# Optimization experiments

Measured on AMD Instinct MI355X. Metric: run time of the kernel, lower is better.

## Reference

```python
import jax, jax.numpy as jnp
import numpy as np
import math

B, N, E, D = 4, 8192, 1024, 64

def setup_inputs() -> dict:
    key = jax.random.key(0)
    kx, kq, kk, kv, ko = jax.random.split(key, 5)
    x = jax.random.normal(kx, (B, N, E), dtype=jnp.float32)
    # ImplicitLinear weights: hash-generated Rademacher-like values scaled by 1/sqrt(in_features).
    # We stand in with sign(normal) * scale, matching the statistics of v_mask_generative * scale.
    wq = jnp.sign(jax.random.normal(kq, (D, E), dtype=jnp.float32)) / math.sqrt(E)
    wk = jnp.sign(jax.random.normal(kk, (D, E), dtype=jnp.float32)) / math.sqrt(E)
    wv = jnp.sign(jax.random.normal(kv, (D, E), dtype=jnp.float32)) / math.sqrt(E)
    wo = jnp.sign(jax.random.normal(ko, (E, D), dtype=jnp.float32)) / math.sqrt(D)
    return {"x": x, "wq": wq, "wk": wk, "wv": wv, "wo": wo}

def reference(x, wq, wk, wv, wo):
    # Projections: ImplicitLinear computes x @ W.T with W shaped [out, in]
    Q = jnp.einsum('bne,de->bnd', x, wq)   # [B,N,D]
    K = jnp.einsum('bne,de->bnd', x, wk)   # [B,N,D]
    V = jnp.einsum('bne,de->bnd', x, wv)   # [B,N,D]
    # ground mode: linear attention, energy = K^T @ V  -> [B,D,D]
    energy = jnp.einsum('bnd,bne->bde', K, V)
    context = jnp.einsum('bnd,bde->bne', Q, energy)  # [B,N,D]
    context = context * jnp.asarray(math.sqrt(3.0 / D), dtype=context.dtype)
    out = jnp.einsum('bnd,ed->bne', context, wo)  # [B,N,E]
    return out
```

## Files before the change

kernel.cpp:

```cpp
#include <hip/hip_runtime.h>
#include <hip/hip_bf16.h>
#include <stdint.h>


typedef __bf16 bf16x8 __attribute__((ext_vector_type(8)));
typedef float  f32x4  __attribute__((ext_vector_type(4)));

#define MFMA_BF16(A, Bb, C) __builtin_amdgcn_mfma_f32_16x16x32_bf16(A, Bb, C, 0, 0, 0)

__device__ __forceinline__ int swz8(int row, int slot) { return (slot ^ (row & 7)) << 3; }

__device__ __forceinline__ void lds_barrier() {
    asm volatile("s_waitcnt lgkmcnt(0)" ::: "memory");
    __builtin_amdgcn_s_barrier();
}

__global__ __launch_bounds__(128) void prep_kernel(
    const float* __restrict__ wq, const float* __restrict__ wk,
    const float* __restrict__ wv, const float* __restrict__ wo,
    __bf16* __restrict__ Wb)
{
    const int gid = blockIdx.x * 128 + threadIdx.x;
    const int e0  = gid * 8;
    const float* src = (e0 < 65536)  ? wq + e0
                     : (e0 < 131072) ? wk + (e0 - 65536)
                     : (e0 < 196608) ? wv + (e0 - 131072)
                                     : wo + (e0 - 196608);
    float w[8];
    *(float4*)&w[0] = *(const float4*)(src);
    *(float4*)&w[4] = *(const float4*)(src + 4);
    bf16x8 wb;
#pragma unroll
    for (int j = 0; j < 8; ++j) wb[j] = (__bf16)w[j];
    *(bf16x8*)&Wb[e0] = wb;
}

__global__ __launch_bounds__(256) void qkv_kernel(
    const float* __restrict__ x, const __bf16* __restrict__ Wb,
    float* __restrict__ Qf, float* __restrict__ Kf, float* __restrict__ Vf)
{
    __shared__ __bf16 xh[2][32 * 64];
    __shared__ __bf16 xl[2][32 * 64];

    const int tid  = threadIdx.x;
    const int lane = tid & 63;
    const int wid  = tid >> 6;
    const int lr   = lane & 15;
    const int kg   = lane >> 4;
    const int row0 = blockIdx.x * 32;
    const int sr   = tid >> 3;
    const int f8   = tid & 7;

    f32x4 acc[2][3];
#pragma unroll
    for (int i = 0; i < 2; ++i)
#pragma unroll
        for (int j = 0; j < 3; ++j) acc[i][j] = (f32x4){0.f, 0.f, 0.f, 0.f};

    const float* xbase = &x[(size_t)(row0 + sr) * 1024 + f8 * 8];
    float xv[8], xn[8], xm[8];
#pragma unroll
    for (int j = 0; j < 8; ++j) xm[j] = 0.f;

#define LOAD_X(dst, stp)                                                       \
    {                                                                          \
        *(float4*)&dst[0] = *(const float4*)(xbase + (stp) * 64);              \
        *(float4*)&dst[4] = *(const float4*)(xbase + (stp) * 64 + 4);          \
    }

    LOAD_X(xv, 0);
    LOAD_X(xn, 1);

    for (int step = 0; step < 16; ++step) {
        const int cur = step & 1;
        {
            bf16x8 h, l;
#pragma unroll
            for (int j = 0; j < 8; ++j) {
                const float v = xv[j];
                const unsigned int bb = __float_as_uint(v);
                h[j] = __builtin_bit_cast(__bf16, (unsigned short)(bb >> 16));
                l[j] = (__bf16)(v - __uint_as_float(bb & 0xffff0000u));
            }
            const int off = sr * 64 + swz8(sr, f8);
            *(bf16x8*)&xh[cur][off] = h;
            *(bf16x8*)&xl[cur][off] = l;
        }
        lds_barrier();
        if (step < 14) LOAD_X(xm, step + 2);

#pragma unroll
        for (int ks = 0; ks < 2; ++ks) {
            const int slot = ks * 4 + kg;
            bf16x8 Ah[2], Al[2], Bw[3];
#pragma unroll
            for (int bn = 0; bn < 3; ++bn) {
                const int col = wid * 48 + bn * 16 + lr;
                Bw[bn] = *(const bf16x8*)&Wb[(size_t)col * 1024 + step * 64 + slot * 8];
            }
#pragma unroll
            for (int am = 0; am < 2; ++am) {
                const int row = am * 16 + lr;
                Ah[am] = *(const bf16x8*)&xh[cur][row * 64 + swz8(row, slot)];
                Al[am] = *(const bf16x8*)&xl[cur][row * 64 + swz8(row, slot)];
            }
#pragma unroll
            for (int am = 0; am < 2; ++am)
#pragma unroll
                for (int bn = 0; bn < 3; ++bn) {
                    acc[am][bn] = MFMA_BF16(Ah[am], Bw[bn], acc[am][bn]);
                    acc[am][bn] = MFMA_BF16(Al[am], Bw[bn], acc[am][bn]);
                }
        }
#pragma unroll
        for (int j = 0; j < 8; ++j) { xv[j] = xn[j]; xn[j] = xm[j]; }
    }
#undef LOAD_X

#pragma unroll
    for (int am = 0; am < 2; ++am)
#pragma unroll
        for (int bn = 0; bn < 3; ++bn) {
            const int col  = wid * 48 + bn * 16 + lr;
            const int rowb = row0 + am * 16 + kg * 4;
            float* dst = (col < 64) ? Qf : (col < 128) ? Kf : Vf;
            const int cc = col & 63;
#pragma unroll
            for (int r = 0; r < 4; ++r)
                dst[(size_t)(rowb + r) * 64 + cc] = acc[am][bn][r];
        }
}

__global__ __launch_bounds__(256) void energy_partial_kernel(
    const float* __restrict__ Kf, const float* __restrict__ Vf,
    float* __restrict__ part)
{
    __shared__ float lK[64 * 64];
    __shared__ float lV[64 * 64];
    const int tid  = threadIdx.x;
    const int row0 = blockIdx.x * 64;

#pragma unroll
    for (int i = 0; i < 4; ++i) {
        const int idx = tid + i * 256;
        const int r   = idx >> 4;
        const int c4  = (idx & 15) << 2;
        *(float4*)&lK[r * 64 + c4] = *(const float4*)&Kf[(size_t)(row0 + r) * 64 + c4];
        *(float4*)&lV[r * 64 + c4] = *(const float4*)&Vf[(size_t)(row0 + r) * 64 + c4];
    }
    __syncthreads();

    const int d  = tid & 63;
    const int eb = (tid >> 6) * 16;
    float acc[16];
#pragma unroll
    for (int j = 0; j < 16; ++j) acc[j] = 0.f;

    for (int n = 0; n < 64; ++n) {
        const float kd = lK[n * 64 + d];
        const float4 v0 = *(const float4*)&lV[n * 64 + eb];
        const float4 v1 = *(const float4*)&lV[n * 64 + eb + 4];
        const float4 v2 = *(const float4*)&lV[n * 64 + eb + 8];
        const float4 v3 = *(const float4*)&lV[n * 64 + eb + 12];
        acc[0]  += kd * v0.x; acc[1]  += kd * v0.y; acc[2]  += kd * v0.z; acc[3]  += kd * v0.w;
        acc[4]  += kd * v1.x; acc[5]  += kd * v1.y; acc[6]  += kd * v1.z; acc[7]  += kd * v1.w;
        acc[8]  += kd * v2.x; acc[9]  += kd * v2.y; acc[10] += kd * v2.z; acc[11] += kd * v2.w;
        acc[12] += kd * v3.x; acc[13] += kd * v3.y; acc[14] += kd * v3.z; acc[15] += kd * v3.w;
    }
    float* p = part + (size_t)blockIdx.x * 4096 + d * 64 + eb;
#pragma unroll
    for (int i = 0; i < 4; ++i)
        *(float4*)&p[i * 4] = make_float4(acc[i*4], acc[i*4+1], acc[i*4+2], acc[i*4+3]);
}

__global__ __launch_bounds__(256) void energy_reduce_kernel(
    const float* __restrict__ part, __bf16* __restrict__ Eth, __bf16* __restrict__ Etl)
{
    const int b    = blockIdx.x >> 4;
    const int elem = ((blockIdx.x & 15) << 8) + threadIdx.x;
    float s = 0.f;
#pragma unroll 8
    for (int c = 0; c < 128; ++c)
        s += part[(size_t)(b * 128 + c) * 4096 + elem];
    s *= 0.2165063509461097f;
    const int d = elem >> 6, e = elem & 63;
    const __bf16 h = (__bf16)s;
    const __bf16 l = (__bf16)(s - (float)h);
    const size_t o = (size_t)b * 4096 + e * 64 + d;
    Eth[o] = h; Etl[o] = l;
}

__global__ __launch_bounds__(256) void ctx_kernel(
    const float* __restrict__ Qf,
    const __bf16* __restrict__ Eth, const __bf16* __restrict__ Etl,
    __bf16* __restrict__ Ch, __bf16* __restrict__ Cl)
{
    __shared__ float ct[4][16 * 68];

    const int tid  = threadIdx.x;
    const int lane = tid & 63;
    const int wid  = tid >> 6;
    const int lr   = lane & 15;
    const int kg   = lane >> 4;
    const int row0 = blockIdx.x * 64 + wid * 16;
    const int b    = blockIdx.x >> 7;

    bf16x8 Qh[2], Ql[2];
#pragma unroll
    for (int ks = 0; ks < 2; ++ks) {
        float qv[8];
        const float* src = &Qf[(size_t)(row0 + lr) * 64 + (ks * 4 + kg) * 8];
        *(float4*)&qv[0] = *(const float4*)(src);
        *(float4*)&qv[4] = *(const float4*)(src + 4);
#pragma unroll
        for (int j = 0; j < 8; ++j) {
            const unsigned int bb = __float_as_uint(qv[j]);
            Qh[ks][j] = __builtin_bit_cast(__bf16, (unsigned short)(bb >> 16));
            Ql[ks][j] = (__bf16)(qv[j] - __uint_as_float(bb & 0xffff0000u));
        }
    }

    f32x4 cacc[4];
#pragma unroll
    for (int i = 0; i < 4; ++i) cacc[i] = (f32x4){0.f, 0.f, 0.f, 0.f};

#pragma unroll
    for (int ks = 0; ks < 2; ++ks) {
        const int slot = ks * 4 + kg;
#pragma unroll
        for (int eb = 0; eb < 4; ++eb) {
            const int e = eb * 16 + lr;
            const bf16x8 Bh = *(const bf16x8*)&Eth[(size_t)b * 4096 + e * 64 + slot * 8];
            const bf16x8 Bl = *(const bf16x8*)&Etl[(size_t)b * 4096 + e * 64 + slot * 8];
            cacc[eb] = MFMA_BF16(Qh[ks], Bh, cacc[eb]);
            cacc[eb] = MFMA_BF16(Qh[ks], Bl, cacc[eb]);
            cacc[eb] = MFMA_BF16(Ql[ks], Bh, cacc[eb]);
        }
    }

#pragma unroll
    for (int eb = 0; eb < 4; ++eb)
#pragma unroll
        for (int r = 0; r < 4; ++r)
            ct[wid][(kg * 4 + r) * 68 + eb * 16 + lr] = cacc[eb][r];
    __syncthreads();

    const int r2 = lane >> 2;
    const int c8 = (lane & 3) * 16;
    float f[16];
#pragma unroll
    for (int i = 0; i < 4; ++i)
        *(float4*)&f[i * 4] = *(const float4*)&ct[wid][r2 * 68 + c8 + i * 4];
    bf16x8 h[2], l[2];
#pragma unroll
    for (int g = 0; g < 2; ++g)
#pragma unroll
        for (int j = 0; j < 8; ++j) {
            const float v = f[g * 8 + j];
            const unsigned int bb = __float_as_uint(v);
            h[g][j] = __builtin_bit_cast(__bf16, (unsigned short)(bb >> 16));
            l[g][j] = (__bf16)(v - __uint_as_float(bb & 0xffff0000u));
        }
    const size_t o = (size_t)(row0 + r2) * 64 + c8;
    *(bf16x8*)&Ch[o]     = h[0];
    *(bf16x8*)&Ch[o + 8] = h[1];
    *(bf16x8*)&Cl[o]     = l[0];
    *(bf16x8*)&Cl[o + 8] = l[1];
}

__global__ __launch_bounds__(256) void out_kernel(
    const __bf16* __restrict__ Ch, const __bf16* __restrict__ Cl,
    const __bf16* __restrict__ Wob, float* __restrict__ out)
{
    const int tid  = threadIdx.x;
    const int lane = tid & 63;
    const int wid  = tid >> 6;
    const int lr   = lane & 15;
    const int kg   = lane >> 4;
    const int row0 = (blockIdx.x >> 1) * 16;
    const int c0   = (blockIdx.x & 1) * 512 + wid * 128;

    bf16x8 Ah[2], Al[2];
#pragma unroll
    for (int ks = 0; ks < 2; ++ks) {
        const size_t o = (size_t)(row0 + lr) * 64 + (ks * 4 + kg) * 8;
        Ah[ks] = *(const bf16x8*)&Ch[o];
        Al[ks] = *(const bf16x8*)&Cl[o];
    }

    f32x4 oacc[8];
#pragma unroll
    for (int i = 0; i < 8; ++i) oacc[i] = (f32x4){0.f, 0.f, 0.f, 0.f};

#pragma unroll
    for (int ks = 0; ks < 2; ++ks) {
        const int slot = ks * 4 + kg;
#pragma unroll
        for (int bn = 0; bn < 8; ++bn) {
            const int col = c0 + bn * 16 + lr;
            const bf16x8 Bw = *(const bf16x8*)&Wob[(size_t)col * 64 + slot * 8];
            oacc[bn] = MFMA_BF16(Ah[ks], Bw, oacc[bn]);
            oacc[bn] = MFMA_BF16(Al[ks], Bw, oacc[bn]);
        }
    }

#pragma unroll
    for (int bn = 0; bn < 8; ++bn)
#pragma unroll
        for (int r = 0; r < 4; ++r)
            __builtin_nontemporal_store(oacc[bn][r],
                &out[(size_t)(row0 + kg * 4 + r) * 1024 + c0 + bn * 16 + lr]);
}

extern "C" void kernel_launch(void* const* d_in, const int* in_sizes, int n_in,
                              void* d_out, int out_size, void* d_ws, size_t ws_size,
                              hipStream_t stream)
{
    const float* x  = (const float*)d_in[0];
    const float* wq = (const float*)d_in[1];
    const float* wk = (const float*)d_in[2];
    const float* wv = (const float*)d_in[3];
    const float* wo = (const float*)d_in[4];
    float* out = (float*)d_out;

    char* ws = (char*)d_ws;
    float*  Qf   = (float*)(ws);
    float*  Kf   = (float*)(ws + 8388608);
    float*  Vf   = (float*)(ws + 16777216);
    float*  part = (float*)(ws + 25165824);
    __bf16* Wb   = (__bf16*)(ws + 33554432);
    __bf16* Wob  = Wb + 196608;
    __bf16* Eth  = (__bf16*)(ws + 34603008);
    __bf16* Etl  = (__bf16*)(ws + 34635776);
    __bf16* Ch   = (__bf16*)(ws + 34668544);
    __bf16* Cl   = (__bf16*)(ws + 38862848);

    prep_kernel<<<256, 128, 0, stream>>>(wq, wk, wv, wo, Wb);
    qkv_kernel<<<1024, 256, 0, stream>>>(x, Wb, Qf, Kf, Vf);
    energy_partial_kernel<<<512, 256, 0, stream>>>(Kf, Vf, part);
    energy_reduce_kernel<<<64, 256, 0, stream>>>(part, Eth, Etl);
    ctx_kernel<<<512, 256, 0, stream>>>(Qf, Eth, Etl, Ch, Cl);
    out_kernel<<<4096, 256, 0, stream>>>(Ch, Cl, Wob, out);
}
```

Before: 338.1 us.

## Fuse context and output projection kernels; rewrite QKV GEMM without LDS staging

```diff
diff --git a/kernel.cpp b/kernel.cpp
--- a/kernel.cpp
+++ b/kernel.cpp
@@ -7,13 +7,6 @@
 typedef float  f32x4  __attribute__((ext_vector_type(4)));
 
 #define MFMA_BF16(A, Bb, C) __builtin_amdgcn_mfma_f32_16x16x32_bf16(A, Bb, C, 0, 0, 0)
-
-__device__ __forceinline__ int swz8(int row, int slot) { return (slot ^ (row & 7)) << 3; }
-
-__device__ __forceinline__ void lds_barrier() {
-    asm volatile("s_waitcnt lgkmcnt(0)" ::: "memory");
-    __builtin_amdgcn_s_barrier();
-}
 
 __global__ __launch_bounds__(128) void prep_kernel(
     const float* __restrict__ wq, const float* __restrict__ wk,
@@ -39,96 +32,79 @@
     const float* __restrict__ x, const __bf16* __restrict__ Wb,
     float* __restrict__ Qf, float* __restrict__ Kf, float* __restrict__ Vf)
 {
-    __shared__ __bf16 xh[2][32 * 64];
-    __shared__ __bf16 xl[2][32 * 64];
-
     const int tid  = threadIdx.x;
     const int lane = tid & 63;
     const int wid  = tid >> 6;
     const int lr   = lane & 15;
     const int kg   = lane >> 4;
-    const int row0 = blockIdx.x * 32;
-    const int sr   = tid >> 3;
-    const int f8   = tid & 7;
-
-    f32x4 acc[2][3];
-#pragma unroll
-    for (int i = 0; i < 2; ++i)
-#pragma unroll
-        for (int j = 0; j < 3; ++j) acc[i][j] = (f32x4){0.f, 0.f, 0.f, 0.f};
-
-    const float* xbase = &x[(size_t)(row0 + sr) * 1024 + f8 * 8];
-    float xv[8], xn[8], xm[8];
-#pragma unroll
-    for (int j = 0; j < 8; ++j) xm[j] = 0.f;
-
-#define LOAD_X(dst, stp)                                                       \
-    {                                                                          \
-        *(float4*)&dst[0] = *(const float4*)(xbase + (stp) * 64);              \
-        *(float4*)&dst[4] = *(const float4*)(xbase + (stp) * 64 + 4);          \
-    }
-
-    LOAD_X(xv, 0);
-    LOAD_X(xn, 1);
-
-    for (int step = 0; step < 16; ++step) {
-        const int cur = step & 1;
-        {
-            bf16x8 h, l;
-#pragma unroll
-            for (int j = 0; j < 8; ++j) {
-                const float v = xv[j];
-                const unsigned int bb = __float_as_uint(v);
-                h[j] = __builtin_bit_cast(__bf16, (unsigned short)(bb >> 16));
-                l[j] = (__bf16)(v - __uint_as_float(bb & 0xffff0000u));
-            }
-            const int off = sr * 64 + swz8(sr, f8);
-            *(bf16x8*)&xh[cur][off] = h;
-            *(bf16x8*)&xl[cur][off] = l;
-        }
-        lds_barrier();
-        if (step < 14) LOAD_X(xm, step + 2);
-
-#pragma unroll
-        for (int ks = 0; ks < 2; ++ks) {
-            const int slot = ks * 4 + kg;
-            bf16x8 Ah[2], Al[2], Bw[3];
-#pragma unroll
-            for (int bn = 0; bn < 3; ++bn) {
-                const int col = wid * 48 + bn * 16 + lr;
-                Bw[bn] = *(const bf16x8*)&Wb[(size_t)col * 1024 + step * 64 + slot * 8];
-            }
-#pragma unroll
-            for (int am = 0; am < 2; ++am) {
-                const int row = am * 16 + lr;
-                Ah[am] = *(const bf16x8*)&xh[cur][row * 64 + swz8(row, slot)];
-                Al[am] = *(const bf16x8*)&xl[cur][row * 64 + swz8(row, slot)];
-            }
-#pragma unroll
-            for (int am = 0; am < 2; ++am)
-#pragma unroll
-                for (int bn = 0; bn < 3; ++bn) {
-                    acc[am][bn] = MFMA_BF16(Ah[am], Bw[bn], acc[am][bn]);
-                    acc[am][bn] = MFMA_BF16(Al[am], Bw[bn], acc[am][bn]);
-                }
-        }
-#pragma unroll
-        for (int j = 0; j < 8; ++j) { xv[j] = xn[j]; xn[j] = xm[j]; }
-    }
-#undef LOAD_X
-
-#pragma unroll
-    for (int am = 0; am < 2; ++am)
-#pragma unroll
-        for (int bn = 0; bn < 3; ++bn) {
-            const int col  = wid * 48 + bn * 16 + lr;
-            const int rowb = row0 + am * 16 + kg * 4;
-            float* dst = (col < 64) ? Qf : (col < 128) ? Kf : Vf;
-            const int cc = col & 63;
-#pragma unroll
-            for (int r = 0; r < 4; ++r)
-                dst[(size_t)(rowb + r) * 64 + cc] = acc[am][bn][r];
-        }
+    const int slab = blockIdx.x >> 1;
+    const int c0   = (blockIdx.x & 1) * 96;
+    const int row0 = slab * 64 + wid * 16;
+
+    const float* xrow = &x[(size_t)(row0 + lr) * 1024 + kg * 8];
+
+    f32x4 acc[6];
+#pragma unroll
+    for (int i = 0; i < 6; ++i) acc[i] = (f32x4){0.f, 0.f, 0.f, 0.f};
+
+    float4 pa0, pa1, qa0, qa1;
+    bf16x8 Bc[6], Bn[6];
+
+#define LOAD_A(B0, B1, STP) {                                                  \
+        const float* ap_ = xrow + (STP) * 32;                                  \
+        B0 = *(const float4*)(ap_);                                            \
+        B1 = *(const float4*)(ap_ + 4); }
+#define LOAD_B(BARR, STP) {                                                    \
+        _Pragma("unroll")                                                      \
+        for (int bn_ = 0; bn_ < 6; ++bn_)                                      \
+            BARR[bn_] = *(const bf16x8*)&Wb[(size_t)(c0 + bn_ * 16 + lr) * 1024 \
+                                            + (STP) * 32 + kg * 8]; }
+#define K1_STEP(S, A0_, A1_, BC, BN) {                                         \
+        if ((S) + 1 < 32) LOAD_B(BN, (S) + 1);                                 \
+        bf16x8 Ah_, Al_;                                                       \
+        const float* fp_ = (const float*)&A0_;                                 \
+        _Pragma("unroll")                                                      \
+        for (int j_ = 0; j_ < 4; ++j_) {                                       \
+            const unsigned int bb_ = __float_as_uint(fp_[j_]);                 \
+            Ah_[j_] = __builtin_bit_cast(__bf16, (unsigned short)(bb_ >> 16)); \
+            Al_[j_] = (__bf16)(fp_[j_] - __uint_as_float(bb_ & 0xffff0000u));  \
+        }                                                                      \
+        const float* gp_ = (const float*)&A1_;                                 \
+        _Pragma("unroll")                                                      \
+        for (int j_ = 0; j_ < 4; ++j_) {                                       \
+            const unsigned int bb_ = __float_as_uint(gp_[j_]);                 \
+            Ah_[4 + j_] = __builtin_bit_cast(__bf16, (unsigned short)(bb_ >> 16)); \
+            Al_[4 + j_] = (__bf16)(gp_[j_] - __uint_as_float(bb_ & 0xffff0000u)); \
+        }                                                                      \
+        if ((S) + 2 < 32) LOAD_A(A0_, A1_, (S) + 2);                           \
+        _Pragma("unroll")                                                      \
+        for (int bn_ = 0; bn_ < 6; ++bn_) {                                    \
+            acc[bn_] = MFMA_BF16(Ah_, BC[bn_], acc[bn_]);                      \
+            acc[bn_] = MFMA_BF16(Al_, BC[bn_], acc[bn_]);                      \
+        } }
+
+    LOAD_A(pa0, pa1, 0);
+    LOAD_A(qa0, qa1, 1);
+    LOAD_B(Bc, 0);
+
+    for (int s = 0; s < 32; s += 2) {
+        K1_STEP(s,     pa0, pa1, Bc, Bn);
+        K1_STEP(s + 1, qa0, qa1, Bn, Bc);
+    }
+#undef LOAD_A
+#undef LOAD_B
+#undef K1_STEP
+
+#pragma unroll
+    for (int bn = 0; bn < 6; ++bn) {
+        const int col  = c0 + bn * 16 + lr;
+        const int rowb = row0 + kg * 4;
+        float* dst = (col < 64) ? Qf : (col < 128) ? Kf : Vf;
+        const int cc = col & 63;
+#pragma unroll
+        for (int r = 0; r < 4; ++r)
+            dst[(size_t)(rowb + r) * 64 + cc] = acc[bn][r];
+    }
 }
 
 __global__ __launch_bounds__(256) void energy_partial_kernel(
@@ -190,10 +166,10 @@
     Eth[o] = h; Etl[o] = l;
 }
 
-__global__ __launch_bounds__(256) void ctx_kernel(
+__global__ __launch_bounds__(256) void out_kernel(
     const float* __restrict__ Qf,
     const __bf16* __restrict__ Eth, const __bf16* __restrict__ Etl,
-    __bf16* __restrict__ Ch, __bf16* __restrict__ Cl)
+    const __bf16* __restrict__ Wob, float* __restrict__ out)
 {
     __shared__ float ct[4][16 * 68];
 
@@ -202,14 +178,16 @@
     const int wid  = tid >> 6;
     const int lr   = lane & 15;
     const int kg   = lane >> 4;
-    const int row0 = blockIdx.x * 64 + wid * 16;
-    const int b    = blockIdx.x >> 7;
+    const int slab = blockIdx.x >> 1;
+    const int c0   = (blockIdx.x & 1) * 512;
+    const int row0 = slab * 64 + wid * 16;
+    const int b    = blockIdx.x >> 8;
 
     bf16x8 Qh[2], Ql[2];
 #pragma unroll
     for (int ks = 0; ks < 2; ++ks) {
         float qv[8];
-        const float* src = &Qf[(size_t)(row0 + lr) * 64 + (ks * 4 + kg) * 8];
+        const float* src = &Qf[(size_t)(row0 + lr) * 64 + ks * 32 + kg * 8];
         *(float4*)&qv[0] = *(const float4*)(src);
         *(float4*)&qv[4] = *(const float4*)(src + 4);
 #pragma unroll
@@ -223,15 +201,13 @@
     f32x4 cacc[4];
 #pragma unroll
     for (int i = 0; i < 4; ++i) cacc[i] = (f32x4){0.f, 0.f, 0.f, 0.f};
-
 #pragma unroll
     for (int ks = 0; ks < 2; ++ks) {
-        const int slot = ks * 4 + kg;
 #pragma unroll
         for (int eb = 0; eb < 4; ++eb) {
             const int e = eb * 16 + lr;
-            const bf16x8 Bh = *(const bf16x8*)&Eth[(size_t)b * 4096 + e * 64 + slot * 8];
-            const bf16x8 Bl = *(const bf16x8*)&Etl[(size_t)b * 4096 + e * 64 + slot * 8];
+            const bf16x8 Bh = *(const bf16x8*)&Eth[(size_t)b * 4096 + e * 64 + ks * 32 + kg * 8];
+            const bf16x8 Bl = *(const bf16x8*)&Etl[(size_t)b * 4096 + e * 64 + ks * 32 + kg * 8];
             cacc[eb] = MFMA_BF16(Qh[ks], Bh, cacc[eb]);
             cacc[eb] = MFMA_BF16(Qh[ks], Bl, cacc[eb]);
             cacc[eb] = MFMA_BF16(Ql[ks], Bh, cacc[eb]);
@@ -243,73 +219,44 @@
 #pragma unroll
         for (int r = 0; r < 4; ++r)
             ct[wid][(kg * 4 + r) * 68 + eb * 16 + lr] = cacc[eb][r];
-    __syncthreads();
-
-    const int r2 = lane >> 2;
-    const int c8 = (lane & 3) * 16;
-    float f[16];
-#pragma unroll
-    for (int i = 0; i < 4; ++i)
-        *(float4*)&f[i * 4] = *(const float4*)&ct[wid][r2 * 68 + c8 + i * 4];
-    bf16x8 h[2], l[2];
-#pragma unroll
-    for (int g = 0; g < 2; ++g)
+    asm volatile("s_waitcnt lgkmcnt(0)" ::: "memory");
+
+    bf16x8 Ah[2], Al[2];
+#pragma unroll
+    for (int ks = 0; ks < 2; ++ks) {
+        float f[8];
+#pragma unroll
+        for (int i = 0; i < 2; ++i)
+            *(float4*)&f[i * 4] = *(const float4*)&ct[wid][lr * 68 + ks * 32 + kg * 8 + i * 4];
 #pragma unroll
         for (int j = 0; j < 8; ++j) {
-            const float v = f[g * 8 + j];
-            const unsigned int bb = __float_as_uint(v);
-            h[g][j] = __builtin_bit_cast(__bf16, (unsigned short)(bb >> 16));
-            l[g][j] = (__bf16)(v - __uint_as_float(bb & 0xffff0000u));
-        }
-    const size_t o = (size_t)(row0 + r2) * 64 + c8;
-    *(bf16x8*)&Ch[o]     = h[0];
-    *(bf16x8*)&Ch[o + 8] = h[1];
-    *(bf16x8*)&Cl[o]     = l[0];
-    *(bf16x8*)&Cl[o + 8] = l[1];
-}
-
-__global__ __launch_bounds__(256) void out_kernel(
-    const __bf16* __restrict__ Ch, const __bf16* __restrict__ Cl,
-    const __bf16* __restrict__ Wob, float* __restrict__ out)
-{
-    const int tid  = threadIdx.x;
-    const int lane = tid & 63;
-    const int wid  = tid >> 6;
-    const int lr   = lane & 15;
-    const int kg   = lane >> 4;
-    const int row0 = (blockIdx.x >> 1) * 16;
-    const int c0   = (blockIdx.x & 1) * 512 + wid * 128;
-
-    bf16x8 Ah[2], Al[2];
-#pragma unroll
-    for (int ks = 0; ks < 2; ++ks) {
-        const size_t o = (size_t)(row0 + lr) * 64 + (ks * 4 + kg) * 8;
-        Ah[ks] = *(const bf16x8*)&Ch[o];
-        Al[ks] = *(const bf16x8*)&Cl[o];
-    }
-
-    f32x4 oacc[8];
-#pragma unroll
-    for (int i = 0; i < 8; ++i) oacc[i] = (f32x4){0.f, 0.f, 0.f, 0.f};
-
-#pragma unroll
-    for (int ks = 0; ks < 2; ++ks) {
-        const int slot = ks * 4 + kg;
-#pragma unroll
-        for (int bn = 0; bn < 8; ++bn) {
-            const int col = c0 + bn * 16 + lr;
-            const bf16x8 Bw = *(const bf16x8*)&Wob[(size_t)col * 64 + slot * 8];
-            oacc[bn] = MFMA_BF16(Ah[ks], Bw, oacc[bn]);
-            oacc[bn] = MFMA_BF16(Al[ks], Bw, oacc[bn]);
-        }
-    }
-
-#pragma unroll
-    for (int bn = 0; bn < 8; ++bn)
-#pragma unroll
-        for (int r = 0; r < 4; ++r)
-            __builtin_nontemporal_store(oacc[bn][r],
-                &out[(size_t)(row0 + kg * 4 + r) * 1024 + c0 + bn * 16 + lr]);
+            const unsigned int bb = __float_as_uint(f[j]);
+            Ah[ks][j] = __builtin_bit_cast(__bf16, (unsigned short)(bb >> 16));
+            Al[ks][j] = (__bf16)(f[j] - __uint_as_float(bb & 0xffff0000u));
+        }
+    }
+
+    for (int g = 0; g < 8; ++g) {
+        f32x4 oacc[4];
+#pragma unroll
+        for (int i = 0; i < 4; ++i) oacc[i] = (f32x4){0.f, 0.f, 0.f, 0.f};
+#pragma unroll
+        for (int ks = 0; ks < 2; ++ks) {
+#pragma unroll
+            for (int bn = 0; bn < 4; ++bn) {
+                const int col = c0 + g * 64 + bn * 16 + lr;
+                const bf16x8 Bw = *(const bf16x8*)&Wob[(size_t)col * 64 + ks * 32 + kg * 8];
+                oacc[bn] = MFMA_BF16(Ah[ks], Bw, oacc[bn]);
+                oacc[bn] = MFMA_BF16(Al[ks], Bw, oacc[bn]);
+            }
+        }
+#pragma unroll
+        for (int bn = 0; bn < 4; ++bn)
+#pragma unroll
+            for (int r = 0; r < 4; ++r)
+                __builtin_nontemporal_store(oacc[bn][r],
+                    &out[(size_t)(row0 + kg * 4 + r) * 1024 + c0 + g * 64 + bn * 16 + lr]);
+    }
 }
 
 extern "C" void kernel_launch(void* const* d_in, const int* in_sizes, int n_in,
@@ -332,13 +279,10 @@
     __bf16* Wob  = Wb + 196608;
     __bf16* Eth  = (__bf16*)(ws + 34603008);
     __bf16* Etl  = (__bf16*)(ws + 34635776);
-    __bf16* Ch   = (__bf16*)(ws + 34668544);
-    __bf16* Cl   = (__bf16*)(ws + 38862848);
 
     prep_kernel<<<256, 128, 0, stream>>>(wq, wk, wv, wo, Wb);
     qkv_kernel<<<1024, 256, 0, stream>>>(x, Wb, Qf, Kf, Vf);
     energy_partial_kernel<<<512, 256, 0, stream>>>(Kf, Vf, part);
     energy_reduce_kernel<<<64, 256, 0, stream>>>(part, Eth, Etl);
-    ctx_kernel<<<512, 256, 0, stream>>>(Qf, Eth, Etl, Ch, Cl);
-    out_kernel<<<4096, 256, 0, stream>>>(Ch, Cl, Wob, out);
-}
+    out_kernel<<<1024, 256, 0, stream>>>(Qf, Eth, Etl, Wob, out);
+}
```

Measured after the change: 362.5 us. 7.2% more time.
